# Kernel tuning notes

Measured on AMD Instinct MI355X. Metric: run time of the kernel, lower is better.

Reference implementation:

```python
import math
import jax, jax.numpy as jnp
import numpy as np

T, E, D = 8192, 64, 2048  # tokens, experts, model_dim


def setup_inputs() -> dict:
    key = jax.random.key(0)
    k1, k2, k3 = jax.random.split(key, 3)
    x = jax.random.normal(k1, (T, D), dtype=jnp.float32)
    wg = jax.random.normal(k2, (E, D), dtype=jnp.float32) * (D ** -0.5)
    # deterministic Gumbel(0,1) noise for second_expert_policy='sampling'
    u = jax.random.uniform(k3, (T, E), dtype=jnp.float32, minval=1e-6, maxval=1.0 - 1e-6)
    gumbel = -jnp.log(-jnp.log(u))
    return {"x": x, "wg": wg, "gumbel": gumbel}


def reference(x, wg, gumbel):
    # logits = wg(input)
    logits = jnp.einsum("td,ed->te", x, wg)  # [T, E]
    gates = jax.nn.softmax(logits, axis=1)
    num_tokens, num_experts = gates.shape
    # training mode: capacity = 2 * ceil(T / E)
    capacity = 2 * math.ceil(num_tokens / num_experts)

    # top-1 expert
    idx1 = jnp.argmax(gates, axis=1)  # [T]
    mask1 = jax.nn.one_hot(idx1, num_experts, dtype=gates.dtype)  # [T, E]

    # second expert: argmax over gumbel-noised logits with top-1 masked out
    logits_except1 = jnp.where(mask1 > 0, -jnp.inf, logits + gumbel)
    idx2 = jnp.argmax(logits_except1, axis=1)
    mask2 = jax.nn.one_hot(idx2, num_experts, dtype=gates.dtype)

    # cumsum-based positions within each expert (fused_cumsum_sub_one)
    locations1 = jnp.cumsum(mask1, axis=0) - 1.0  # [T, E]
    locations2 = jnp.cumsum(mask2, axis=0) - 1.0 + jnp.sum(mask1, axis=0, keepdims=True)

    # load-balancing auxiliary loss
    me = jnp.mean(gates, axis=0)
    ce = jnp.mean(mask1, axis=0)
    l_aux = jnp.mean(me * ce) * num_experts * num_experts

    # drop tokens over capacity
    mask1 = mask1 * (locations1 < capacity).astype(mask1.dtype)
    mask2 = mask2 * (locations2 < capacity).astype(mask2.dtype)

    # gate values, normalized after dropping
    gates1_s = jnp.sum(gates * mask1, axis=1)
    gates2_s = jnp.sum(gates * mask2, axis=1)
    denom = jnp.maximum(gates1_s + gates2_s, jnp.finfo(jnp.float32).eps)
    gates1_s = gates1_s / denom
    gates2_s = gates2_s / denom

    loc1_s = jnp.sum(locations1 * mask1, axis=1).astype(jnp.int32)  # [T]
    loc2_s = jnp.sum(locations2 * mask2, axis=1).astype(jnp.int32)

    gates1 = gates1_s[:, None] * mask1  # [T, E]
    gates2 = gates2_s[:, None] * mask2
    loc1_sc = jax.nn.one_hot(loc1_s, capacity, dtype=gates.dtype)  # [T, C]
    loc2_sc = jax.nn.one_hot(loc2_s, capacity, dtype=gates.dtype)

    # combine weights: outer product over (expert, capacity) per token
    combine_weights = gates1[:, :, None] * loc1_sc[:, None, :] + gates2[:, :, None] * loc2_sc[:, None, :]
    dispatch_mask = combine_weights > 0
    return l_aux, combine_weights, dispatch_mask
```

## Files before the change

### kernel.cpp

```cpp
#include <hip/hip_runtime.h>
#include <cstdint>
#include <cstddef>

#define T_TOK 8192
#define NE    64
#define ND    2048
#define CAP   256

#define GEMM_B 128
#define ZB     4096

__global__ __launch_bounds__(128) void kA(
    const float* __restrict__ x, const float* __restrict__ wg,
    const float* __restrict__ gum,
    int* __restrict__ idx1o, int* __restrict__ idx2o,
    float* __restrict__ g1o, float* __restrict__ g2o,
    float* __restrict__ meb,
    float4* __restrict__ o4, long n4, float* __restrict__ o, long n) {
  __shared__ float xs[64][68];
  __shared__ float wt[64][68];
  __shared__ float mred[2][64];

  if (blockIdx.x >= GEMM_B) {
    long i = (long)(blockIdx.x - GEMM_B) * 128 + threadIdx.x;
    const long stride = (long)ZB * 128;
    const float4 z = make_float4(0.f, 0.f, 0.f, 0.f);
    for (; i < n4; i += stride) o4[i] = z;
    if (blockIdx.x == GEMM_B && threadIdx.x == 0) {
      for (long j = n4 * 4; j < n; ++j) o[j] = 0.f;
    }
    return;
  }

  const int tid = threadIdx.x;
  const int t0 = blockIdx.x * 64;
  const int tg8 = (tid >> 4) << 3;
  const int eg4 = (tid & 15) << 2;

  float acc[8][4];
#pragma unroll
  for (int i = 0; i < 8; ++i)
#pragma unroll
    for (int j = 0; j < 4; ++j) acc[i][j] = 0.f;

  for (int kt = 0; kt < ND; kt += 64) {
#pragma unroll
    for (int it = 0; it < 8; ++it) {
      const int j = tid + it * 128;
      const int r = j >> 4;
      const int cb = (j & 15) << 2;
      const int sw = ((cb >> 2) & 7) << 2;
      const int rs = r ^ sw;
      float4 vx = *reinterpret_cast<const float4*>(x + (size_t)(t0 + r) * ND + kt + cb);
      xs[cb + 0][rs] = vx.x; xs[cb + 1][rs] = vx.y;
      xs[cb + 2][rs] = vx.z; xs[cb + 3][rs] = vx.w;
      float4 vw = *reinterpret_cast<const float4*>(wg + (size_t)r * ND + kt + cb);
      wt[cb + 0][rs] = vw.x; wt[cb + 1][rs] = vw.y;
      wt[cb + 2][rs] = vw.z; wt[cb + 3][rs] = vw.w;
    }
    __syncthreads();
#pragma unroll 4
    for (int k = 0; k < 64; ++k) {
      const int s = ((k >> 2) & 7) << 2;
      float4 a0 = *reinterpret_cast<const float4*>(&xs[k][tg8 ^ s]);
      float4 a1 = *reinterpret_cast<const float4*>(&xs[k][(tg8 + 4) ^ s]);
      float4 b  = *reinterpret_cast<const float4*>(&wt[k][eg4 ^ s]);
      float av[8] = {a0.x, a0.y, a0.z, a0.w, a1.x, a1.y, a1.z, a1.w};
      float bv[4] = {b.x, b.y, b.z, b.w};
#pragma unroll
      for (int i = 0; i < 8; ++i)
#pragma unroll
        for (int j = 0; j < 4; ++j) acc[i][j] = fmaf(av[i], bv[j], acc[i][j]);
    }
    __syncthreads();
  }

  float* lgp = &xs[0][0];
#pragma unroll
  for (int i = 0; i < 8; ++i) {
    float4 v = make_float4(acc[i][0], acc[i][1], acc[i][2], acc[i][3]);
    *reinterpret_cast<float4*>(lgp + (size_t)(tg8 + i) * 68 + eg4) = v;
  }
  __syncthreads();

  const int wave = tid >> 6;
  const int lane = tid & 63;
  float meacc = 0.f;
  for (int i = 0; i < 32; ++i) {
    const int tt = wave * 32 + i;
    const int t = t0 + tt;
    const float logit = lgp[tt * 68 + lane];
    float m = logit;
#pragma unroll
    for (int o2 = 32; o2; o2 >>= 1) m = fmaxf(m, __shfl_xor(m, o2));
    const float ex = expf(logit - m);
    float s = ex;
#pragma unroll
    for (int o2 = 32; o2; o2 >>= 1) s += __shfl_xor(s, o2);
    const float gate = ex / s;
    meacc += gate;
    float v1 = logit; int i1 = lane;
#pragma unroll
    for (int o2 = 32; o2; o2 >>= 1) {
      float vv = __shfl_xor(v1, o2); int jj = __shfl_xor(i1, o2);
      if (vv > v1 || (vv == v1 && jj < i1)) { v1 = vv; i1 = jj; }
    }
    float v2 = (lane == i1) ? -__builtin_inff() : logit + gum[(size_t)t * NE + lane];
    int i2 = lane;
#pragma unroll
    for (int o2 = 32; o2; o2 >>= 1) {
      float vv = __shfl_xor(v2, o2); int jj = __shfl_xor(i2, o2);
      if (vv > v2 || (vv == v2 && jj < i2)) { v2 = vv; i2 = jj; }
    }
    const float gv1 = __shfl(gate, i1);
    const float gv2 = __shfl(gate, i2);
    if (lane == 0) {
      idx1o[t] = i1; idx2o[t] = i2; g1o[t] = gv1; g2o[t] = gv2;
    }
  }
  mred[wave][lane] = meacc;
  __syncthreads();
  if (tid < 64) meb[(size_t)blockIdx.x * NE + tid] = mred[0][tid] + mred[1][tid];
}

__global__ __launch_bounds__(256) void k_scan(
    const int* __restrict__ idx1, const int* __restrict__ idx2,
    int* __restrict__ loc1, int* __restrict__ loc2, int* __restrict__ cnt1) {
  const int e = blockIdx.x;
  const int tid = threadIdx.x;
  const int base = tid * 32;
  int c1 = 0, c2 = 0;
  for (int i = 0; i < 32; ++i) {
    c1 += (idx1[base + i] == e);
    c2 += (idx2[base + i] == e);
  }
  const int lane = tid & 63, wave = tid >> 6;
  int s1 = c1, s2 = c2;
#pragma unroll
  for (int o = 1; o < 64; o <<= 1) {
    int t1 = __shfl_up(s1, o), t2 = __shfl_up(s2, o);
    if (lane >= o) { s1 += t1; s2 += t2; }
  }
  __shared__ int wt1[4], wt2[4];
  if (lane == 63) { wt1[wave] = s1; wt2[wave] = s2; }
  __syncthreads();
  int off1 = 0, off2 = 0, tot1 = 0;
#pragma unroll
  for (int w = 0; w < 4; ++w) {
    tot1 += wt1[w];
    if (w < wave) { off1 += wt1[w]; off2 += wt2[w]; }
  }
  int p1 = off1 + s1 - c1;
  int p2 = off2 + s2 - c2 + tot1;
  for (int i = 0; i < 32; ++i) {
    if (idx1[base + i] == e) loc1[base + i] = p1++;
    if (idx2[base + i] == e) loc2[base + i] = p2++;
  }
  if (tid == 0) cnt1[e] = tot1;
}

__global__ __launch_bounds__(256) void k_scat(
    const int* __restrict__ idx1, const int* __restrict__ idx2,
    const float* __restrict__ g1, const float* __restrict__ g2,
    const int* __restrict__ loc1, const int* __restrict__ loc2,
    const float* __restrict__ meb, const int* __restrict__ cnt1,
    float* __restrict__ out) {
  if (blockIdx.x == T_TOK / 256) {
    const int lane = threadIdx.x;
    if (lane >= 64) return;
    float ms = 0.f;
    for (int b = 0; b < GEMM_B; ++b) ms += meb[(size_t)b * NE + lane];
    const float me = ms / (float)T_TOK;
    const float ce = (float)cnt1[lane] / (float)T_TOK;
    float v = me * ce;
#pragma unroll
    for (int o = 32; o; o >>= 1) v += __shfl_xor(v, o);
    if (lane == 0) out[0] = v * (float)NE;
    return;
  }
  const int t = blockIdx.x * 256 + threadIdx.x;
  const int l1 = loc1[t], l2 = loc2[t];
  const bool k1 = l1 < CAP, k2 = l2 < CAP;
  const float a = k1 ? g1[t] : 0.f;
  const float b = k2 ? g2[t] : 0.f;
  const float denom = fmaxf(a + b, 1.1920929e-07f);
  float* cw = out + 1;
  float* dm = out + 1 + (size_t)T_TOK * NE * CAP;
  if (k1) {
    size_t o = ((size_t)t * NE + idx1[t]) * CAP + l1;
    cw[o] = a / denom; dm[o] = 1.0f;
  }
  if (k2) {
    size_t o = ((size_t)t * NE + idx2[t]) * CAP + l2;
    cw[o] = b / denom; dm[o] = 1.0f;
  }
}

extern "C" void kernel_launch(void* const* d_in, const int* in_sizes, int n_in,
                              void* d_out, int out_size, void* d_ws, size_t ws_size,
                              hipStream_t stream) {
  const float* x   = (const float*)d_in[0];
  const float* wg  = (const float*)d_in[1];
  const float* gum = (const float*)d_in[2];
  float* out = (float*)d_out;

  char* ws = (char*)d_ws;
  int*   idx1 = (int*)(ws + 0);
  int*   idx2 = (int*)(ws + 32768);
  float* g1   = (float*)(ws + 65536);
  float* g2   = (float*)(ws + 98304);
  int*   loc1 = (int*)(ws + 131072);
  int*   loc2 = (int*)(ws + 163840);
  int*   cnt1 = (int*)(ws + 196608);
  float* meb  = (float*)(ws + 196864);

  const long n  = (long)out_size;
  const long n4 = n >> 2;

  kA<<<dim3(GEMM_B + ZB), dim3(128), 0, stream>>>(
      x, wg, gum, idx1, idx2, g1, g2, meb, (float4*)out, n4, out, n);
  k_scan<<<dim3(NE), dim3(256), 0, stream>>>(idx1, idx2, loc1, loc2, cnt1);
  k_scat<<<dim3(T_TOK / 256 + 1), dim3(256), 0, stream>>>(
      idx1, idx2, g1, g2, loc1, loc2, meb, cnt1, out);
}
```

Measured before the change: 364.2 us.

## Split GEMM K-dimension across waves with 8x8 register tiles and reduce

Each of the two waves in a GEMM block now handles half of the reduction dimension in its own shared-memory tiles, computing a full 64x64 logits tile with an 8x8 per-thread accumulator. The partial sums are combined through shared memory before the softmax/top-2 stage. Tiles are stored row-major with direct float4 stores instead of transposed swizzled scalar stores, so staging becomes simpler. In exchange the accumulator doubles to 64 registers, row strides of 68 may cause LDS bank conflicts on the float4 reads, and shared memory use doubles.

```diff
diff --git a/kernel.cpp b/kernel.cpp
--- a/kernel.cpp
+++ b/kernel.cpp
@@ -8,7 +8,7 @@
 #define CAP   256
 
 #define GEMM_B 128
-#define ZB     4096
+#define FB     4096
 
 __global__ __launch_bounds__(128) void kA(
     const float* __restrict__ x, const float* __restrict__ wg,
@@ -17,13 +17,13 @@
     float* __restrict__ g1o, float* __restrict__ g2o,
     float* __restrict__ meb,
     float4* __restrict__ o4, long n4, float* __restrict__ o, long n) {
-  __shared__ float xs[64][68];
-  __shared__ float wt[64][68];
+  __shared__ float sA[2][64][68];
+  __shared__ float sB[2][64][68];
   __shared__ float mred[2][64];
 
   if (blockIdx.x >= GEMM_B) {
     long i = (long)(blockIdx.x - GEMM_B) * 128 + threadIdx.x;
-    const long stride = (long)ZB * 128;
+    const long stride = (long)FB * 128;
     const float4 z = make_float4(0.f, 0.f, 0.f, 0.f);
     for (; i < n4; i += stride) o4[i] = z;
     if (blockIdx.x == GEMM_B && threadIdx.x == 0) {
@@ -32,64 +32,76 @@
     return;
   }
 
-  const int tid = threadIdx.x;
-  const int t0 = blockIdx.x * 64;
-  const int tg8 = (tid >> 4) << 3;
-  const int eg4 = (tid & 15) << 2;
-
-  float acc[8][4];
+  const int tid  = threadIdx.x;
+  const int wv   = tid >> 6;
+  const int lane = tid & 63;
+  const int r    = lane >> 3;
+  const int c    = lane & 7;
+  const int t0   = blockIdx.x * 64;
+  const int k0   = wv * (ND / 2);
+
+  float acc[8][8];
 #pragma unroll
   for (int i = 0; i < 8; ++i)
 #pragma unroll
-    for (int j = 0; j < 4; ++j) acc[i][j] = 0.f;
-
-  for (int kt = 0; kt < ND; kt += 64) {
-#pragma unroll
-    for (int it = 0; it < 8; ++it) {
-      const int j = tid + it * 128;
-      const int r = j >> 4;
-      const int cb = (j & 15) << 2;
-      const int sw = ((cb >> 2) & 7) << 2;
-      const int rs = r ^ sw;
-      float4 vx = *reinterpret_cast<const float4*>(x + (size_t)(t0 + r) * ND + kt + cb);
-      xs[cb + 0][rs] = vx.x; xs[cb + 1][rs] = vx.y;
-      xs[cb + 2][rs] = vx.z; xs[cb + 3][rs] = vx.w;
-      float4 vw = *reinterpret_cast<const float4*>(wg + (size_t)r * ND + kt + cb);
-      wt[cb + 0][rs] = vw.x; wt[cb + 1][rs] = vw.y;
-      wt[cb + 2][rs] = vw.z; wt[cb + 3][rs] = vw.w;
+    for (int j = 0; j < 8; ++j) acc[i][j] = 0.f;
+
+  for (int kt = k0; kt < k0 + ND / 2; kt += 64) {
+#pragma unroll
+    for (int it = 0; it < 16; ++it) {
+      const int idx = it * 64 + lane;
+      const int row = idx >> 4;
+      const int k4  = (idx & 15) << 2;
+      *reinterpret_cast<float4*>(&sA[wv][row][k4]) =
+          *reinterpret_cast<const float4*>(x + (size_t)(t0 + row) * ND + kt + k4);
+      *reinterpret_cast<float4*>(&sB[wv][row][k4]) =
+          *reinterpret_cast<const float4*>(wg + (size_t)row * ND + kt + k4);
     }
     __syncthreads();
-#pragma unroll 4
-    for (int k = 0; k < 64; ++k) {
-      const int s = ((k >> 2) & 7) << 2;
-      float4 a0 = *reinterpret_cast<const float4*>(&xs[k][tg8 ^ s]);
-      float4 a1 = *reinterpret_cast<const float4*>(&xs[k][(tg8 + 4) ^ s]);
-      float4 b  = *reinterpret_cast<const float4*>(&wt[k][eg4 ^ s]);
-      float av[8] = {a0.x, a0.y, a0.z, a0.w, a1.x, a1.y, a1.z, a1.w};
-      float bv[4] = {b.x, b.y, b.z, b.w};
+#pragma unroll 1
+    for (int k4 = 0; k4 < 64; k4 += 4) {
+      float4 xa[8], wb[8];
+#pragma unroll
+      for (int j = 0; j < 8; ++j)
+        xa[j] = *reinterpret_cast<const float4*>(&sA[wv][8 * j + r][k4]);
+#pragma unroll
+      for (int j = 0; j < 8; ++j)
+        wb[j] = *reinterpret_cast<const float4*>(&sB[wv][8 * j + c][k4]);
 #pragma unroll
       for (int i = 0; i < 8; ++i)
 #pragma unroll
-        for (int j = 0; j < 4; ++j) acc[i][j] = fmaf(av[i], bv[j], acc[i][j]);
+        for (int j = 0; j < 8; ++j) {
+          acc[i][j] = fmaf(xa[i].x, wb[j].x, acc[i][j]);
+          acc[i][j] = fmaf(xa[i].y, wb[j].y, acc[i][j]);
+          acc[i][j] = fmaf(xa[i].z, wb[j].z, acc[i][j]);
+          acc[i][j] = fmaf(xa[i].w, wb[j].w, acc[i][j]);
+        }
     }
     __syncthreads();
   }
 
-  float* lgp = &xs[0][0];
-#pragma unroll
-  for (int i = 0; i < 8; ++i) {
-    float4 v = make_float4(acc[i][0], acc[i][1], acc[i][2], acc[i][3]);
-    *reinterpret_cast<float4*>(lgp + (size_t)(tg8 + i) * 68 + eg4) = v;
-  }
-  __syncthreads();
-
-  const int wave = tid >> 6;
-  const int lane = tid & 63;
+  if (wv == 1) {
+#pragma unroll
+    for (int i = 0; i < 8; ++i)
+#pragma unroll
+      for (int j = 0; j < 8; ++j) sA[1][8 * i + r][8 * j + c] = acc[i][j];
+  }
+  __syncthreads();
+  if (wv == 0) {
+#pragma unroll
+    for (int i = 0; i < 8; ++i)
+#pragma unroll
+      for (int j = 0; j < 8; ++j)
+        sA[0][8 * i + r][8 * j + c] = acc[i][j] + sA[1][8 * i + r][8 * j + c];
+  }
+  __syncthreads();
+
+  const float* lg = &sA[0][0][0];
   float meacc = 0.f;
-  for (int i = 0; i < 32; ++i) {
-    const int tt = wave * 32 + i;
+  for (int ii = 0; ii < 32; ++ii) {
+    const int tt = wv * 32 + ii;
     const int t = t0 + tt;
-    const float logit = lgp[tt * 68 + lane];
+    const float logit = lg[tt * 68 + lane];
     float m = logit;
 #pragma unroll
     for (int o2 = 32; o2; o2 >>= 1) m = fmaxf(m, __shfl_xor(m, o2));
@@ -118,7 +130,7 @@
       idx1o[t] = i1; idx2o[t] = i2; g1o[t] = gv1; g2o[t] = gv2;
     }
   }
-  mred[wave][lane] = meacc;
+  mred[wv][lane] = meacc;
   __syncthreads();
   if (tid < 64) meb[(size_t)blockIdx.x * NE + tid] = mred[0][tid] + mred[1][tid];
 }
@@ -217,7 +229,7 @@
   const long n  = (long)out_size;
   const long n4 = n >> 2;
 
-  kA<<<dim3(GEMM_B + ZB), dim3(128), 0, stream>>>(
+  kA<<<dim3(GEMM_B + FB), dim3(128), 0, stream>>>(
       x, wg, gum, idx1, idx2, g1, g2, meb, (float4*)out, n4, out, n);
   k_scan<<<dim3(NE), dim3(256), 0, stream>>>(idx1, idx2, loc1, loc2, cnt1);
   k_scat<<<dim3(T_TOK / 256 + 1), dim3(256), 0, stream>>>(
```

New measurement: 554.8 us. 52.3% more time.

## Replace LDS-tiled gating GEMM with per-lane register dot products

Applied to the files above, without the earlier changes.

Rewrites the gating GEMM so each 64-thread block handles 32 tokens, and each lane pair splits the 64 experts into two halves. Each lane streams its x row and the wg rows straight from global memory into 32 register accumulators. This removes the LDS staging and barriers, and softmax, top-1 and top-2 are done per lane with one cross-lane shuffle. The zero-fill block count is retuned to match. The cost is much less data reuse: x rows are read with strided, poorly coalesced accesses and wg is re-read by every wave, relying on cache.

```diff
diff --git a/kernel.cpp b/kernel.cpp
--- a/kernel.cpp
+++ b/kernel.cpp
@@ -7,120 +7,129 @@
 #define ND    2048
 #define CAP   256
 
-#define GEMM_B 128
-#define ZB     4096
-
-__global__ __launch_bounds__(128) void kA(
+#define GEMM_B 256
+#define FB     3840
+
+__global__ __launch_bounds__(64) void kA(
     const float* __restrict__ x, const float* __restrict__ wg,
     const float* __restrict__ gum,
     int* __restrict__ idx1o, int* __restrict__ idx2o,
     float* __restrict__ g1o, float* __restrict__ g2o,
     float* __restrict__ meb,
     float4* __restrict__ o4, long n4, float* __restrict__ o, long n) {
-  __shared__ float xs[64][68];
-  __shared__ float wt[64][68];
-  __shared__ float mred[2][64];
+  const int lane = threadIdx.x;
 
   if (blockIdx.x >= GEMM_B) {
-    long i = (long)(blockIdx.x - GEMM_B) * 128 + threadIdx.x;
-    const long stride = (long)ZB * 128;
+    long i = (long)(blockIdx.x - GEMM_B) * 64 + lane;
+    const long stride = (long)FB * 64;
     const float4 z = make_float4(0.f, 0.f, 0.f, 0.f);
     for (; i < n4; i += stride) o4[i] = z;
-    if (blockIdx.x == GEMM_B && threadIdx.x == 0) {
+    if (blockIdx.x == GEMM_B && lane == 0) {
       for (long j = n4 * 4; j < n; ++j) o[j] = 0.f;
     }
     return;
   }
 
-  const int tid = threadIdx.x;
-  const int t0 = blockIdx.x * 64;
-  const int tg8 = (tid >> 4) << 3;
-  const int eg4 = (tid & 15) << 2;
-
-  float acc[8][4];
-#pragma unroll
-  for (int i = 0; i < 8; ++i)
-#pragma unroll
-    for (int j = 0; j < 4; ++j) acc[i][j] = 0.f;
-
-  for (int kt = 0; kt < ND; kt += 64) {
-#pragma unroll
-    for (int it = 0; it < 8; ++it) {
-      const int j = tid + it * 128;
-      const int r = j >> 4;
-      const int cb = (j & 15) << 2;
-      const int sw = ((cb >> 2) & 7) << 2;
-      const int rs = r ^ sw;
-      float4 vx = *reinterpret_cast<const float4*>(x + (size_t)(t0 + r) * ND + kt + cb);
-      xs[cb + 0][rs] = vx.x; xs[cb + 1][rs] = vx.y;
-      xs[cb + 2][rs] = vx.z; xs[cb + 3][rs] = vx.w;
-      float4 vw = *reinterpret_cast<const float4*>(wg + (size_t)r * ND + kt + cb);
-      wt[cb + 0][rs] = vw.x; wt[cb + 1][rs] = vw.y;
-      wt[cb + 2][rs] = vw.z; wt[cb + 3][rs] = vw.w;
-    }
-    __syncthreads();
-#pragma unroll 4
-    for (int k = 0; k < 64; ++k) {
-      const int s = ((k >> 2) & 7) << 2;
-      float4 a0 = *reinterpret_cast<const float4*>(&xs[k][tg8 ^ s]);
-      float4 a1 = *reinterpret_cast<const float4*>(&xs[k][(tg8 + 4) ^ s]);
-      float4 b  = *reinterpret_cast<const float4*>(&wt[k][eg4 ^ s]);
-      float av[8] = {a0.x, a0.y, a0.z, a0.w, a1.x, a1.y, a1.z, a1.w};
-      float bv[4] = {b.x, b.y, b.z, b.w};
-#pragma unroll
-      for (int i = 0; i < 8; ++i)
-#pragma unroll
-        for (int j = 0; j < 4; ++j) acc[i][j] = fmaf(av[i], bv[j], acc[i][j]);
-    }
-    __syncthreads();
-  }
-
-  float* lgp = &xs[0][0];
-#pragma unroll
-  for (int i = 0; i < 8; ++i) {
-    float4 v = make_float4(acc[i][0], acc[i][1], acc[i][2], acc[i][3]);
-    *reinterpret_cast<float4*>(lgp + (size_t)(tg8 + i) * 68 + eg4) = v;
-  }
-  __syncthreads();
-
-  const int wave = tid >> 6;
-  const int lane = tid & 63;
-  float meacc = 0.f;
-  for (int i = 0; i < 32; ++i) {
-    const int tt = wave * 32 + i;
-    const int t = t0 + tt;
-    const float logit = lgp[tt * 68 + lane];
-    float m = logit;
-#pragma unroll
-    for (int o2 = 32; o2; o2 >>= 1) m = fmaxf(m, __shfl_xor(m, o2));
-    const float ex = expf(logit - m);
-    float s = ex;
-#pragma unroll
-    for (int o2 = 32; o2; o2 >>= 1) s += __shfl_xor(s, o2);
-    const float gate = ex / s;
-    meacc += gate;
-    float v1 = logit; int i1 = lane;
-#pragma unroll
-    for (int o2 = 32; o2; o2 >>= 1) {
-      float vv = __shfl_xor(v1, o2); int jj = __shfl_xor(i1, o2);
-      if (vv > v1 || (vv == v1 && jj < i1)) { v1 = vv; i1 = jj; }
-    }
-    float v2 = (lane == i1) ? -__builtin_inff() : logit + gum[(size_t)t * NE + lane];
-    int i2 = lane;
-#pragma unroll
-    for (int o2 = 32; o2; o2 >>= 1) {
-      float vv = __shfl_xor(v2, o2); int jj = __shfl_xor(i2, o2);
-      if (vv > v2 || (vv == v2 && jj < i2)) { v2 = vv; i2 = jj; }
-    }
-    const float gv1 = __shfl(gate, i1);
-    const float gv2 = __shfl(gate, i2);
-    if (lane == 0) {
-      idx1o[t] = i1; idx2o[t] = i2; g1o[t] = gv1; g2o[t] = gv2;
-    }
-  }
-  mred[wave][lane] = meacc;
-  __syncthreads();
-  if (tid < 64) meb[(size_t)blockIdx.x * NE + tid] = mred[0][tid] + mred[1][tid];
+  const int tr = lane >> 1;
+  const int eh = lane & 1;
+  const int t  = blockIdx.x * 32 + tr;
+  const float* __restrict__ xr = x + (size_t)t * ND;
+  const float* __restrict__ wr = wg + (size_t)eh * 32 * ND;
+
+  float acc[32];
+#pragma unroll
+  for (int j = 0; j < 32; ++j) acc[j] = 0.f;
+
+  for (int k = 0; k < ND; k += 16) {
+    float4 xv[4];
+#pragma unroll
+    for (int q = 0; q < 4; ++q)
+      xv[q] = *reinterpret_cast<const float4*>(xr + k + 4 * q);
+#pragma unroll
+    for (int g = 0; g < 8; ++g) {
+      const float* __restrict__ wb = wr + (size_t)(g * 4) * ND + k;
+#pragma unroll
+      for (int q = 0; q < 4; ++q) {
+        float4 w0 = *reinterpret_cast<const float4*>(wb + 0 * ND + 4 * q);
+        float4 w1 = *reinterpret_cast<const float4*>(wb + 1 * ND + 4 * q);
+        float4 w2 = *reinterpret_cast<const float4*>(wb + 2 * ND + 4 * q);
+        float4 w3 = *reinterpret_cast<const float4*>(wb + 3 * ND + 4 * q);
+        const float4 xq = xv[q];
+        acc[g*4+0] = fmaf(xq.x, w0.x, fmaf(xq.y, w0.y, fmaf(xq.z, w0.z, fmaf(xq.w, w0.w, acc[g*4+0]))));
+        acc[g*4+1] = fmaf(xq.x, w1.x, fmaf(xq.y, w1.y, fmaf(xq.z, w1.z, fmaf(xq.w, w1.w, acc[g*4+1]))));
+        acc[g*4+2] = fmaf(xq.x, w2.x, fmaf(xq.y, w2.y, fmaf(xq.z, w2.z, fmaf(xq.w, w2.w, acc[g*4+2]))));
+        acc[g*4+3] = fmaf(xq.x, w3.x, fmaf(xq.y, w3.y, fmaf(xq.z, w3.z, fmaf(xq.w, w3.w, acc[g*4+3]))));
+      }
+    }
+  }
+
+  float m = acc[0];
+#pragma unroll
+  for (int j = 1; j < 32; ++j) m = fmaxf(m, acc[j]);
+  m = fmaxf(m, __shfl_xor(m, 1));
+  float s = 0.f;
+#pragma unroll
+  for (int j = 0; j < 32; ++j) s += expf(acc[j] - m);
+  s += __shfl_xor(s, 1);
+
+  float v1 = acc[0]; int j1 = 0;
+#pragma unroll
+  for (int j = 1; j < 32; ++j)
+    if (acc[j] > v1) { v1 = acc[j]; j1 = j; }
+  int i1 = eh * 32 + j1;
+  {
+    float vp = __shfl_xor(v1, 1); int ip = __shfl_xor(i1, 1);
+    const bool mine = eh == 0 ? (v1 >= vp) : (v1 > vp);
+    v1 = mine ? v1 : vp; i1 = mine ? i1 : ip;
+  }
+
+  float gv[32];
+  {
+    const float4* gp = reinterpret_cast<const float4*>(gum + (size_t)t * NE + eh * 32);
+#pragma unroll
+    for (int q = 0; q < 8; ++q) {
+      float4 g4 = gp[q];
+      gv[q*4+0] = g4.x; gv[q*4+1] = g4.y; gv[q*4+2] = g4.z; gv[q*4+3] = g4.w;
+    }
+  }
+  float v2 = -__builtin_inff(); int j2 = 0;
+#pragma unroll
+  for (int j = 0; j < 32; ++j) {
+    float w = (eh * 32 + j == i1) ? -__builtin_inff() : acc[j] + gv[j];
+    if (w > v2) { v2 = w; j2 = j; }
+  }
+  int i2 = eh * 32 + j2;
+  {
+    float vq = __shfl_xor(v2, 1); int iq = __shfl_xor(i2, 1);
+    const bool mine = eh == 0 ? (v2 >= vq) : (v2 > vq);
+    i2 = mine ? i2 : iq;
+  }
+
+#pragma unroll
+  for (int j = 0; j < 32; ++j) acc[j] = expf(acc[j] - m) / s;
+
+  float gl1 = ((i1 >> 5) == eh) ? acc[i1 & 31] : 0.f;
+  const float g1v = gl1 + __shfl_xor(gl1, 1);
+  float gl2 = ((i2 >> 5) == eh) ? acc[i2 & 31] : 0.f;
+  const float g2v = gl2 + __shfl_xor(gl2, 1);
+
+  if (eh == 0) {
+    idx1o[t] = i1; idx2o[t] = i2; g1o[t] = g1v; g2o[t] = g2v;
+  }
+
+#pragma unroll
+  for (int d = 2; d < 64; d <<= 1)
+#pragma unroll
+    for (int j = 0; j < 32; ++j) acc[j] += __shfl_xor(acc[j], d);
+
+  if (tr == 0) {
+    float* mrow = meb + (size_t)blockIdx.x * NE + eh * 32;
+#pragma unroll
+    for (int j = 0; j < 32; j += 4) {
+      float4 v = make_float4(acc[j], acc[j+1], acc[j+2], acc[j+3]);
+      *reinterpret_cast<float4*>(mrow + j) = v;
+    }
+  }
 }
 
 __global__ __launch_bounds__(256) void k_scan(
@@ -212,12 +221,12 @@
   int*   loc1 = (int*)(ws + 131072);
   int*   loc2 = (int*)(ws + 163840);
   int*   cnt1 = (int*)(ws + 196608);
-  float* meb  = (float*)(ws + 196864);
+  float* meb  = (float*)(ws + 197120);
 
   const long n  = (long)out_size;
   const long n4 = n >> 2;
 
-  kA<<<dim3(GEMM_B + ZB), dim3(128), 0, stream>>>(
+  kA<<<dim3(GEMM_B + FB), dim3(64), 0, stream>>>(
       x, wg, gum, idx1, idx2, g1, g2, meb, (float4*)out, n4, out, n);
   k_scan<<<dim3(NE), dim3(256), 0, stream>>>(idx1, idx2, loc1, loc2, cnt1);
   k_scat<<<dim3(T_TOK / 256 + 1), dim3(256), 0, stream>>>(
```

After: 703.1 us. 1.93x slower.
